# Performance work log

Hardware: AMD Instinct MI355X
Metric: run time of the kernel (lower is better)

## Reference

```python
import jax, jax.numpy as jnp
import numpy as np

B, S, D = 4, 2048, 1024
H = 16
HD = D // H  # 64


def setup_inputs() -> dict:
    key = jax.random.key(0)
    ks = jax.random.split(key, 4)
    scale = 0.02
    return {
        "hidden_states": jax.random.normal(ks[0], (B, S, D), dtype=jnp.float32),
        "attention_mask": jnp.zeros((B, 1, 1, S), dtype=jnp.float32),
        "Wq": jax.random.normal(ks[1], (D, D), dtype=jnp.float32) * scale,
        "bq": jnp.zeros((D,), dtype=jnp.float32),
        "Wk": jax.random.normal(ks[2], (D, D), dtype=jnp.float32) * scale,
        "bk": jnp.zeros((D,), dtype=jnp.float32),
        "Wv": jax.random.normal(ks[3], (D, D), dtype=jnp.float32) * scale,
        "bv": jnp.zeros((D,), dtype=jnp.float32),
    }


def reference(hidden_states, attention_mask, Wq, bq, Wk, bk, Wv, bv):
    # linear projections: x @ W^T + b (torch nn.Linear convention); here W stored as [D,D]
    def proj(x, W, b):
        y = jnp.einsum("bsd,ed->bse", x, W) + b
        # [B,S,D] -> [B,H,S,HD]
        return y.reshape(B, S, H, HD).transpose(0, 2, 1, 3)

    q = proj(hidden_states, Wq, bq)
    k = proj(hidden_states, Wk, bk)
    v = proj(hidden_states, Wv, bv)

    scores = jnp.einsum("bhqd,bhkd->bhqk", q, k) / jnp.sqrt(jnp.float32(HD))
    scores = scores + attention_mask  # additive mask broadcast [B,1,1,S]
    probs = jax.nn.softmax(scores, axis=-1)  # dropout p=0 -> identity
    ctx = jnp.einsum("bhqk,bhkd->bhqd", probs, v)
    ctx = ctx.transpose(0, 2, 1, 3).reshape(B, S, D)
    return ctx
```

## Files before the change

### kernel.cpp

```cpp
#include <hip/hip_runtime.h>
#include <hip/hip_bf16.h>

typedef __attribute__((ext_vector_type(4))) float f32x4;
typedef __attribute__((ext_vector_type(8))) short bf16x8;
typedef __attribute__((ext_vector_type(8))) unsigned short u16x8;
typedef unsigned short u16;

#define DEV static __device__ __forceinline__

DEV u16 f2bf(float f) {
    union { float f; unsigned int u; } v; v.f = f;
    unsigned int r = v.u + 0x7FFFu + ((v.u >> 16) & 1u);
    return (u16)(r >> 16);
}

DEV unsigned int cvt_pk(float lo, float hi) {
    unsigned int r;
    asm("v_cvt_pk_bf16_f32 %0, %1, %2" : "=v"(r) : "v"(lo), "v"(hi));
    return r;
}

DEV void async16(const void* g, void* l) {
    __builtin_amdgcn_global_load_lds((const __attribute__((address_space(1))) unsigned int*)g,
                                     (__attribute__((address_space(3))) unsigned int*)l, 16, 0, 0);
}

__global__ void cvt_all(const float4* __restrict__ x, const float4* __restrict__ wq,
                        const float4* __restrict__ wk, const float4* __restrict__ wv,
                        ushort4* __restrict__ xb, ushort4* __restrict__ wb) {
    int bid = blockIdx.x;
    const float4* s;
    ushort4* d;
    int i;
    if (bid < 8192) {
        s = x; d = xb; i = bid * 256 + threadIdx.x;
    } else {
        int r = bid - 8192;
        int wsel = r >> 10;
        s = (wsel == 0) ? wq : (wsel == 1) ? wk : wv;
        d = wb + (size_t)wsel * 262144;
        i = (r & 1023) * 256 + threadIdx.x;
    }
    float4 v = s[i];
    ushort4 o;
    o.x = f2bf(v.x); o.y = f2bf(v.y); o.z = f2bf(v.z); o.w = f2bf(v.w);
    d[i] = o;
}

__launch_bounds__(256, 2)
__global__ void qkv_gemm(const u16* __restrict__ xb, const u16* __restrict__ wb,
                         const float* __restrict__ bq, const float* __restrict__ bk,
                         const float* __restrict__ bv,
                         u16* __restrict__ Qb, u16* __restrict__ Kb, u16* __restrict__ Vtb) {
    __shared__ u16 Al[2][128 * 64];
    __shared__ u16 Bl[2][128 * 64];
    const int t = threadIdx.x, ln = t & 63, w = t >> 6;
    const int wr = w >> 1, wc = w & 1;
    const int m0 = blockIdx.x * 128, e0 = blockIdx.y * 128, p = blockIdx.z;
    const u16* Wp = wb + (size_t)p * 1048576;
    const float* bias = (p == 0) ? bq : (p == 1) ? bk : bv;

    const int srow = t >> 3, scol = (t & 7) * 8;

    f32x4 acc[4][4];
#pragma unroll
    for (int i = 0; i < 4; i++)
#pragma unroll
        for (int j = 0; j < 4; j++) acc[i][j] = (f32x4){0.f, 0.f, 0.f, 0.f};

#define G_STAGE(buf, kk)                                                              \
    {                                                                                 \
        _Pragma("unroll")                                                             \
        for (int c = 0; c < 4; c++) {                                                 \
            int r = c * 32 + srow;                                                    \
            async16(&xb[(size_t)(m0 + r) * 1024 + (kk) + scol], &Al[buf][r * 64 + scol]); \
            async16(&Wp[(size_t)(e0 + r) * 1024 + (kk) + scol], &Bl[buf][r * 64 + scol]); \
        }                                                                             \
    }

    G_STAGE(0, 0);
    __syncthreads();
    int cur = 0;
    for (int kt = 0; kt < 16; kt++) {
        if (kt < 15) G_STAGE(cur ^ 1, (kt + 1) * 64);
#pragma unroll
        for (int kc = 0; kc < 2; kc++) {
            bf16x8 a[4], bb[4];
#pragma unroll
            for (int mf = 0; mf < 4; mf++)
                a[mf] = *(const bf16x8*)&Al[cur][(wr * 64 + mf * 16 + (ln & 15)) * 64 + kc * 32 + (ln >> 4) * 8];
#pragma unroll
            for (int nf = 0; nf < 4; nf++)
                bb[nf] = *(const bf16x8*)&Bl[cur][(wc * 64 + nf * 16 + (ln & 15)) * 64 + kc * 32 + (ln >> 4) * 8];
            __builtin_amdgcn_s_setprio(1);
#pragma unroll
            for (int mf = 0; mf < 4; mf++)
#pragma unroll
                for (int nf = 0; nf < 4; nf++)
                    acc[mf][nf] = __builtin_amdgcn_mfma_f32_16x16x32_bf16(a[mf], bb[nf], acc[mf][nf], 0, 0, 0);
            __builtin_amdgcn_s_setprio(0);
        }
        __syncthreads();
        cur ^= 1;
    }
#undef G_STAGE

    const int q16 = ln & 15, g = ln >> 4;
    if (p == 2) {
#pragma unroll
        for (int nf = 0; nf < 4; nf++) {
            int e = e0 + wc * 64 + nf * 16 + q16;
            float bias_v = bias[e];
            int h = e >> 6, hd = e & 63;
#pragma unroll
            for (int mf = 0; mf < 4; mf++) {
                int m = m0 + wr * 64 + mf * 16 + g * 4;
                int b = m >> 11, s = m & 2047;
                ushort4 pk;
                pk.x = f2bf(acc[mf][nf][0] + bias_v);
                pk.y = f2bf(acc[mf][nf][1] + bias_v);
                pk.z = f2bf(acc[mf][nf][2] + bias_v);
                pk.w = f2bf(acc[mf][nf][3] + bias_v);
                *(ushort4*)&Vtb[((size_t)((b * 16 + h) * 64 + hd)) * 2048 + s] = pk;
            }
        }
    } else {
        u16* out = (p == 0) ? Qb : Kb;
#pragma unroll
        for (int nf = 0; nf < 4; nf++) {
            int e = e0 + wc * 64 + nf * 16 + q16;
            float bias_v = bias[e];
            int h = e >> 6, hd = e & 63;
#pragma unroll
            for (int mf = 0; mf < 4; mf++) {
#pragma unroll
                for (int r = 0; r < 4; r++) {
                    int m = m0 + wr * 64 + mf * 16 + g * 4 + r;
                    int b = m >> 11, s = m & 2047;
                    out[((size_t)(b * 16 + h) * 2048 + s) * 64 + hd] = f2bf(acc[mf][nf][r] + bias_v);
                }
            }
        }
    }
}

__launch_bounds__(256, 3)
__global__ void attn_kernel(const u16* __restrict__ Q, const u16* __restrict__ K,
                            const u16* __restrict__ Vt, const float* __restrict__ mask,
                            float* __restrict__ out) {
    __shared__ u16 Kl[2][64 * 64];
    __shared__ u16 Vl[2][64 * 64];
    __shared__ u16 Pl[4][32 * 64];
    const int t = threadIdx.x, ln = t & 63, w = t >> 6;
    const int q16 = ln & 15, g = ln >> 4;

    const int bid0 = blockIdx.x;
    const int swz = (bid0 & 7) * 128 + (bid0 >> 3);
    const int qbi = swz & 15, bh = swz >> 4;
    const int b = bh >> 4, h = bh & 15;
    const int qr = qbi * 128 + w * 32;
    const size_t base = (size_t)bh * 2048 * 64;
    const float L2E = 1.44269504088896340736f;
    const float C1 = 0.125f * L2E;

    bf16x8 aq[2][2];
#pragma unroll
    for (int mf = 0; mf < 2; mf++)
#pragma unroll
        for (int dc = 0; dc < 2; dc++)
            aq[mf][dc] = *(const bf16x8*)&Q[base + (size_t)(qr + mf * 16 + q16) * 64 + dc * 32 + g * 8];

    const int row0 = t >> 3, row1 = 32 + (t >> 3);
    const int sc = (t & 7) ^ (row0 & 7);

    const int swz0 = (g ^ (q16 & 7)) * 8;
    const int swz1 = ((g ^ 4) ^ (q16 & 7)) * 8;

#define A_STAGE(buf, kk)                                                              \
    {                                                                                 \
        async16(&K[base + (size_t)((kk) + row0) * 64 + sc * 8], &Kl[buf][t * 8]);     \
        async16(&K[base + (size_t)((kk) + row1) * 64 + sc * 8], &Kl[buf][2048 + t * 8]); \
        async16(&Vt[base + (size_t)row0 * 2048 + (kk) + sc * 8], &Vl[buf][t * 8]);    \
        async16(&Vt[base + (size_t)row1 * 2048 + (kk) + sc * 8], &Vl[buf][2048 + t * 8]); \
    }

    f32x4 accT[4][2];
    f32x4 lacc[2];
#pragma unroll
    for (int nf = 0; nf < 4; nf++)
#pragma unroll
        for (int mf = 0; mf < 2; mf++) accT[nf][mf] = (f32x4){0.f, 0.f, 0.f, 0.f};
    lacc[0] = (f32x4){0.f, 0.f, 0.f, 0.f};
    lacc[1] = (f32x4){0.f, 0.f, 0.f, 0.f};

    A_STAGE(0, 0);
    __syncthreads();
    int cur = 0;

    for (int kt = 0; kt < 32; kt++) {
        const int k0 = kt * 64;
        if (kt < 31) A_STAGE(cur ^ 1, k0 + 64);

        f32x4 st[4][2];
        __builtin_amdgcn_s_setprio(1);
#pragma unroll
        for (int kf = 0; kf < 4; kf++) {
            bf16x8 ka0 = *(const bf16x8*)&Kl[cur][(kf * 16 + q16) * 64 + swz0];
            bf16x8 ka1 = *(const bf16x8*)&Kl[cur][(kf * 16 + q16) * 64 + swz1];
#pragma unroll
            for (int mf = 0; mf < 2; mf++) {
                f32x4 z = (f32x4){0.f, 0.f, 0.f, 0.f};
                z = __builtin_amdgcn_mfma_f32_16x16x32_bf16(ka0, aq[mf][0], z, 0, 0, 0);
                z = __builtin_amdgcn_mfma_f32_16x16x32_bf16(ka1, aq[mf][1], z, 0, 0, 0);
                st[kf][mf] = z;
            }
        }
        __builtin_amdgcn_s_setprio(0);

        f32x4 mv4[4];
#pragma unroll
        for (int kf = 0; kf < 4; kf++)
            mv4[kf] = *(const f32x4*)&mask[(size_t)b * 2048 + k0 + kf * 16 + g * 4];

#pragma unroll
        for (int mf = 0; mf < 2; mf++) {
#pragma unroll
            for (int kf = 0; kf < 4; kf++) {
#pragma unroll
                for (int r = 0; r < 4; r++)
                    st[kf][mf][r] = __builtin_amdgcn_exp2f(st[kf][mf][r] * C1 + mv4[kf][r] * L2E);
            }
            lacc[mf] += (st[0][mf] + st[1][mf]) + (st[2][mf] + st[3][mf]);
#pragma unroll
            for (int kf = 0; kf < 4; kf++) {
                uint2 pk;
                pk.x = cvt_pk(st[kf][mf][0], st[kf][mf][1]);
                pk.y = cvt_pk(st[kf][mf][2], st[kf][mf][3]);
                *(uint2*)&Pl[w][(mf * 16 + q16) * 64 + ((kf * 16 + g * 4) ^ ((q16 & 7) << 3))] = pk;
            }
        }

        __builtin_amdgcn_s_setprio(1);
#pragma unroll
        for (int kc = 0; kc < 2; kc++) {
            const int so = kc ? swz1 : swz0;
            bf16x8 pa[2], bv4[4];
#pragma unroll
            for (int mf = 0; mf < 2; mf++)
                pa[mf] = *(const bf16x8*)&Pl[w][(mf * 16 + q16) * 64 + so];
#pragma unroll
            for (int nf = 0; nf < 4; nf++)
                bv4[nf] = *(const bf16x8*)&Vl[cur][(nf * 16 + q16) * 64 + so];
#pragma unroll
            for (int nf = 0; nf < 4; nf++)
#pragma unroll
                for (int mf = 0; mf < 2; mf++)
                    accT[nf][mf] = __builtin_amdgcn_mfma_f32_16x16x32_bf16(bv4[nf], pa[mf], accT[nf][mf], 0, 0, 0);
        }
        __builtin_amdgcn_s_setprio(0);

        __syncthreads();
        cur ^= 1;
    }
#undef A_STAGE

#pragma unroll
    for (int mf = 0; mf < 2; mf++) {
        float l = (lacc[mf][0] + lacc[mf][1]) + (lacc[mf][2] + lacc[mf][3]);
        l += __shfl_xor(l, 16);
        l += __shfl_xor(l, 32);
        float inv = 1.0f / l;
        int q = qr + mf * 16 + q16;
#pragma unroll
        for (int nf = 0; nf < 4; nf++) {
            f32x4 o = accT[nf][mf] * inv;
            *(f32x4*)&out[((size_t)(b * 2048 + q)) * 1024 + h * 64 + nf * 16 + g * 4] = o;
        }
    }
}

extern "C" void kernel_launch(void* const* d_in, const int* in_sizes, int n_in,
                              void* d_out, int out_size, void* d_ws, size_t ws_size,
                              hipStream_t stream) {
    const float* x    = (const float*)d_in[0];
    const float* mask = (const float*)d_in[1];
    const float* Wq   = (const float*)d_in[2];
    const float* bq   = (const float*)d_in[3];
    const float* Wk   = (const float*)d_in[4];
    const float* bk   = (const float*)d_in[5];
    const float* Wv   = (const float*)d_in[6];
    const float* bv   = (const float*)d_in[7];
    float* out = (float*)d_out;

    char* ws = (char*)d_ws;
    if (ws_size < (size_t)73400320) return;
    u16* xb  = (u16*)(ws);
    u16* wb  = (u16*)(ws + 16777216);
    u16* Qb  = (u16*)(ws + 23068672);
    u16* Kb  = (u16*)(ws + 39845888);
    u16* Vtb = (u16*)(ws + 56623104);

    cvt_all<<<11264, 256, 0, stream>>>((const float4*)x, (const float4*)Wq, (const float4*)Wk,
                                       (const float4*)Wv, (ushort4*)xb, (ushort4*)wb);
    qkv_gemm<<<dim3(64, 8, 3), 256, 0, stream>>>(xb, wb, bq, bk, bv, Qb, Kb, Vtb);
    attn_kernel<<<1024, 256, 0, stream>>>(Qb, Kb, Vtb, mask, out);
}
```

Baseline: 193.3 us.

## Fold exp(mask) into V and row-sum, process query fragments sequentially

Precomputes exp(mask) once in the conversion kernel and multiplies it into V in the QKV GEMM epilogue and into the softmax denominator, so the attention inner loop drops the per-element mask FMA. The attention loop is restructured to handle one 16-row query fragment at a time, halving the P staging buffer and live score registers. Launch bounds are raised to 4 blocks per SU to gain occupancy. The risks are bf16 rounding of mask-scaled V (a large negative mask gives zero V instead of a masked score) and possible register spills at the higher occupancy.

After: 196.1 us. About the same (+1.4%).

```diff
diff --git a/kernel.cpp b/kernel.cpp
--- a/kernel.cpp
+++ b/kernel.cpp
@@ -27,8 +27,14 @@
 
 __global__ void cvt_all(const float4* __restrict__ x, const float4* __restrict__ wq,
                         const float4* __restrict__ wk, const float4* __restrict__ wv,
-                        ushort4* __restrict__ xb, ushort4* __restrict__ wb) {
+                        ushort4* __restrict__ xb, ushort4* __restrict__ wb,
+                        const float* __restrict__ mask, float* __restrict__ em) {
     int bid = blockIdx.x;
+    if (bid >= 11264) {
+        int i = (bid - 11264) * 256 + threadIdx.x;
+        em[i] = __builtin_amdgcn_exp2f(mask[i] * 1.44269504088896340736f);
+        return;
+    }
     const float4* s;
     ushort4* d;
     int i;
@@ -50,7 +56,7 @@
 __launch_bounds__(256, 2)
 __global__ void qkv_gemm(const u16* __restrict__ xb, const u16* __restrict__ wb,
                          const float* __restrict__ bq, const float* __restrict__ bk,
-                         const float* __restrict__ bv,
+                         const float* __restrict__ bv, const float* __restrict__ em,
                          u16* __restrict__ Qb, u16* __restrict__ Kb, u16* __restrict__ Vtb) {
     __shared__ u16 Al[2][128 * 64];
     __shared__ u16 Bl[2][128 * 64];
@@ -116,11 +122,12 @@
             for (int mf = 0; mf < 4; mf++) {
                 int m = m0 + wr * 64 + mf * 16 + g * 4;
                 int b = m >> 11, s = m & 2047;
+                f32x4 emv = *(const f32x4*)&em[b * 2048 + s];
                 ushort4 pk;
-                pk.x = f2bf(acc[mf][nf][0] + bias_v);
-                pk.y = f2bf(acc[mf][nf][1] + bias_v);
-                pk.z = f2bf(acc[mf][nf][2] + bias_v);
-                pk.w = f2bf(acc[mf][nf][3] + bias_v);
+                pk.x = f2bf((acc[mf][nf][0] + bias_v) * emv[0]);
+                pk.y = f2bf((acc[mf][nf][1] + bias_v) * emv[1]);
+                pk.z = f2bf((acc[mf][nf][2] + bias_v) * emv[2]);
+                pk.w = f2bf((acc[mf][nf][3] + bias_v) * emv[3]);
                 *(ushort4*)&Vtb[((size_t)((b * 16 + h) * 64 + hd)) * 2048 + s] = pk;
             }
         }
@@ -144,13 +151,13 @@
     }
 }
 
-__launch_bounds__(256, 3)
+__launch_bounds__(256, 4)
 __global__ void attn_kernel(const u16* __restrict__ Q, const u16* __restrict__ K,
-                            const u16* __restrict__ Vt, const float* __restrict__ mask,
+                            const u16* __restrict__ Vt, const float* __restrict__ em,
                             float* __restrict__ out) {
     __shared__ u16 Kl[2][64 * 64];
     __shared__ u16 Vl[2][64 * 64];
-    __shared__ u16 Pl[4][32 * 64];
+    __shared__ u16 Pl[4][16 * 64];
     const int t = threadIdx.x, ln = t & 63, w = t >> 6;
     const int q16 = ln & 15, g = ln >> 4;
 
@@ -201,63 +208,63 @@
         const int k0 = kt * 64;
         if (kt < 31) A_STAGE(cur ^ 1, k0 + 64);
 
-        f32x4 st[4][2];
-        __builtin_amdgcn_s_setprio(1);
+        f32x4 em4[4];
+#pragma unroll
+        for (int kf = 0; kf < 4; kf++)
+            em4[kf] = *(const f32x4*)&em[b * 2048 + k0 + kf * 16 + g * 4];
+
+        bf16x8 ka[4][2];
 #pragma unroll
         for (int kf = 0; kf < 4; kf++) {
-            bf16x8 ka0 = *(const bf16x8*)&Kl[cur][(kf * 16 + q16) * 64 + swz0];
-            bf16x8 ka1 = *(const bf16x8*)&Kl[cur][(kf * 16 + q16) * 64 + swz1];
-#pragma unroll
-            for (int mf = 0; mf < 2; mf++) {
+            ka[kf][0] = *(const bf16x8*)&Kl[cur][(kf * 16 + q16) * 64 + swz0];
+            ka[kf][1] = *(const bf16x8*)&Kl[cur][(kf * 16 + q16) * 64 + swz1];
+        }
+
+#pragma unroll
+        for (int mf = 0; mf < 2; mf++) {
+            f32x4 st[4];
+            __builtin_amdgcn_s_setprio(1);
+#pragma unroll
+            for (int kf = 0; kf < 4; kf++) {
                 f32x4 z = (f32x4){0.f, 0.f, 0.f, 0.f};
-                z = __builtin_amdgcn_mfma_f32_16x16x32_bf16(ka0, aq[mf][0], z, 0, 0, 0);
-                z = __builtin_amdgcn_mfma_f32_16x16x32_bf16(ka1, aq[mf][1], z, 0, 0, 0);
-                st[kf][mf] = z;
-            }
-        }
-        __builtin_amdgcn_s_setprio(0);
-
-        f32x4 mv4[4];
-#pragma unroll
-        for (int kf = 0; kf < 4; kf++)
-            mv4[kf] = *(const f32x4*)&mask[(size_t)b * 2048 + k0 + kf * 16 + g * 4];
-
-#pragma unroll
-        for (int mf = 0; mf < 2; mf++) {
-#pragma unroll
-            for (int kf = 0; kf < 4; kf++) {
+                z = __builtin_amdgcn_mfma_f32_16x16x32_bf16(ka[kf][0], aq[mf][0], z, 0, 0, 0);
+                z = __builtin_amdgcn_mfma_f32_16x16x32_bf16(ka[kf][1], aq[mf][1], z, 0, 0, 0);
+                st[kf] = z;
+            }
+            __builtin_amdgcn_s_setprio(0);
+
+#pragma unroll
+            for (int kf = 0; kf < 4; kf++)
 #pragma unroll
                 for (int r = 0; r < 4; r++)
-                    st[kf][mf][r] = __builtin_amdgcn_exp2f(st[kf][mf][r] * C1 + mv4[kf][r] * L2E);
-            }
-            lacc[mf] += (st[0][mf] + st[1][mf]) + (st[2][mf] + st[3][mf]);
+                    st[kf][r] = __builtin_amdgcn_exp2f(st[kf][r] * C1);
+#pragma unroll
+            for (int kf = 0; kf < 4; kf++)
+                lacc[mf] += st[kf] * em4[kf];
+
 #pragma unroll
             for (int kf = 0; kf < 4; kf++) {
                 uint2 pk;
-                pk.x = cvt_pk(st[kf][mf][0], st[kf][mf][1]);
-                pk.y = cvt_pk(st[kf][mf][2], st[kf][mf][3]);
-                *(uint2*)&Pl[w][(mf * 16 + q16) * 64 + ((kf * 16 + g * 4) ^ ((q16 & 7) << 3))] = pk;
-            }
-        }
-
-        __builtin_amdgcn_s_setprio(1);
-#pragma unroll
-        for (int kc = 0; kc < 2; kc++) {
-            const int so = kc ? swz1 : swz0;
-            bf16x8 pa[2], bv4[4];
-#pragma unroll
-            for (int mf = 0; mf < 2; mf++)
-                pa[mf] = *(const bf16x8*)&Pl[w][(mf * 16 + q16) * 64 + so];
-#pragma unroll
-            for (int nf = 0; nf < 4; nf++)
-                bv4[nf] = *(const bf16x8*)&Vl[cur][(nf * 16 + q16) * 64 + so];
-#pragma unroll
-            for (int nf = 0; nf < 4; nf++)
-#pragma unroll
-                for (int mf = 0; mf < 2; mf++)
-                    accT[nf][mf] = __builtin_amdgcn_mfma_f32_16x16x32_bf16(bv4[nf], pa[mf], accT[nf][mf], 0, 0, 0);
-        }
-        __builtin_amdgcn_s_setprio(0);
+                pk.x = cvt_pk(st[kf][0], st[kf][1]);
+                pk.y = cvt_pk(st[kf][2], st[kf][3]);
+                *(uint2*)&Pl[w][q16 * 64 + ((kf * 16 + g * 4) ^ ((q16 & 7) << 3))] = pk;
+            }
+
+            __builtin_amdgcn_s_setprio(1);
+#pragma unroll
+            for (int kc = 0; kc < 2; kc++) {
+                const int so = kc ? swz1 : swz0;
+                bf16x8 pa = *(const bf16x8*)&Pl[w][q16 * 64 + so];
+                bf16x8 bv4[4];
+#pragma unroll
+                for (int nf = 0; nf < 4; nf++)
+                    bv4[nf] = *(const bf16x8*)&Vl[cur][(nf * 16 + q16) * 64 + so];
+#pragma unroll
+                for (int nf = 0; nf < 4; nf++)
+                    accT[nf][mf] = __builtin_amdgcn_mfma_f32_16x16x32_bf16(bv4[nf], pa, accT[nf][mf], 0, 0, 0);
+            }
+            __builtin_amdgcn_s_setprio(0);
+        }
 
         __syncthreads();
         cur ^= 1;
@@ -293,15 +300,16 @@
     float* out = (float*)d_out;
 
     char* ws = (char*)d_ws;
-    if (ws_size < (size_t)73400320) return;
-    u16* xb  = (u16*)(ws);
-    u16* wb  = (u16*)(ws + 16777216);
-    u16* Qb  = (u16*)(ws + 23068672);
-    u16* Kb  = (u16*)(ws + 39845888);
-    u16* Vtb = (u16*)(ws + 56623104);
-
-    cvt_all<<<11264, 256, 0, stream>>>((const float4*)x, (const float4*)Wq, (const float4*)Wk,
-                                       (const float4*)Wv, (ushort4*)xb, (ushort4*)wb);
-    qkv_gemm<<<dim3(64, 8, 3), 256, 0, stream>>>(xb, wb, bq, bk, bv, Qb, Kb, Vtb);
-    attn_kernel<<<1024, 256, 0, stream>>>(Qb, Kb, Vtb, mask, out);
-}
+    if (ws_size < (size_t)73433088) return;
+    u16* xb   = (u16*)(ws);
+    u16* wb   = (u16*)(ws + 16777216);
+    u16* Qb   = (u16*)(ws + 23068672);
+    u16* Kb   = (u16*)(ws + 39845888);
+    u16* Vtb  = (u16*)(ws + 56623104);
+    float* em = (float*)(ws + 73400320);
+
+    cvt_all<<<11296, 256, 0, stream>>>((const float4*)x, (const float4*)Wq, (const float4*)Wk,
+                                       (const float4*)Wv, (ushort4*)xb, (ushort4*)wb, mask, em);
+    qkv_gemm<<<dim3(64, 8, 3), 256, 0, stream>>>(xb, wb, bq, bk, bv, em, Qb, Kb, Vtb);
+    attn_kernel<<<1024, 256, 0, stream>>>(Qb, Kb, Vtb, em, out);
+}
```
